# Kernel optimization log

Hardware: AMD Instinct MI355X
Metric: run time of the kernel (lower is better)

## Reference

```python
import jax, jax.numpy as jnp
import numpy as np

N = 50000      # nodes
E = 800000     # edges (avg degree 16)
F_IN = 100     # num_node_features
H = 64         # hidden
C = 18         # num_class
L = 2          # num_layers (extra GINConv blocks after first_conv)
BN_EPS = 1e-5


def setup_inputs() -> dict:
    key = jax.random.key(0)
    ks = jax.random.split(key, 12)
    s = 0.05  # weight init scale
    return {
        "x": jax.random.normal(ks[0], (N, F_IN), dtype=jnp.float32),
        "edge_index": jax.random.randint(ks[1], (2, E), 0, N, dtype=jnp.int32),
        # learnable eps per GINConv (train_eps=True, init 0): [first, layer0, layer1]
        "eps": jnp.zeros((L + 1,), jnp.float32),
        # first_conv MLP: Linear(F_IN,H) -> ReLU -> Linear(H,H)
        "fW1": jax.random.normal(ks[2], (F_IN, H), jnp.float32) * s,
        "fb1": jnp.zeros((H,), jnp.float32),
        "fW2": jax.random.normal(ks[3], (H, H), jnp.float32) * s,
        "fb2": jnp.zeros((H,), jnp.float32),
        # per-layer MLPs, stacked over L layers
        "W1s": jax.random.normal(ks[4], (L, H, H), jnp.float32) * s,
        "b1s": jnp.zeros((L, H), jnp.float32),
        "W2s": jax.random.normal(ks[5], (L, H, H), jnp.float32) * s,
        "b2s": jnp.zeros((L, H), jnp.float32),
        # BatchNorm1d params for first_bn + L bns (eval mode: running stats)
        "bn_gamma": jnp.ones((L + 1, H), jnp.float32),
        "bn_beta": jnp.zeros((L + 1, H), jnp.float32),
        "bn_mean": jnp.zeros((L + 1, H), jnp.float32),
        "bn_var": jnp.ones((L + 1, H), jnp.float32),
        # readout linears
        "lin1_W": jax.random.normal(ks[6], (H, H), jnp.float32) * s,
        "lin1_b": jnp.zeros((H,), jnp.float32),
        "lin2_W": jax.random.normal(ks[7], (H, C), jnp.float32) * s,
        "lin2_b": jnp.zeros((C,), jnp.float32),
    }


def _mlp(h, W1, b1, W2, b2):
    return jnp.maximum(h @ W1 + b1, 0.0) @ W2 + b2


def _gin_conv(x, src, dst, eps, W1, b1, W2, b2):
    # sum aggregation of source features into destination nodes
    agg = jax.ops.segment_sum(x[src], dst, num_segments=N)  # [N, d]
    return _mlp((1.0 + eps) * x + agg, W1, b1, W2, b2)


def _bn_eval(h, g, b, m, v):
    return (h - m) * jax.lax.rsqrt(v + BN_EPS) * g + b


def reference(x, edge_index, eps, fW1, fb1, fW2, fb2, W1s, b1s, W2s, b2s,
              bn_gamma, bn_beta, bn_mean, bn_var, lin1_W, lin1_b, lin2_W, lin2_b):
    src, dst = edge_index[0], edge_index[1]
    h = jnp.maximum(_gin_conv(x, src, dst, eps[0], fW1, fb1, fW2, fb2), 0.0)
    h = _bn_eval(h, bn_gamma[0], bn_beta[0], bn_mean[0], bn_var[0])
    for i in range(L):
        h = jnp.maximum(_gin_conv(h, src, dst, eps[i + 1],
                                  W1s[i], b1s[i], W2s[i], b2s[i]), 0.0)
        h = _bn_eval(h, bn_gamma[i + 1], bn_beta[i + 1], bn_mean[i + 1], bn_var[i + 1])
    h = jnp.maximum(h @ lin1_W + lin1_b, 0.0)
    # dropout is identity in eval mode
    h = h @ lin2_W + lin2_b
    return jax.nn.log_softmax(h, axis=-1)
```

## Files before the change

kernel.cpp:

```cpp
#include <hip/hip_runtime.h>
#include <math.h>

#define NN 50000
#define EE 800000
#define FIN 100
#define HH 64
#define CC 18
#define PD 68
#define TB 782
#define NB 49

__global__ __launch_bounds__(256) void k_count(const int* __restrict__ ei,
                                               int* __restrict__ counts) {
  for (int e = blockIdx.x * 256 + threadIdx.x; e < EE; e += gridDim.x * 256)
    atomicAdd(&counts[ei[EE + e]], 1);
}

__device__ __forceinline__ void load4_guard(const int* __restrict__ a, int i4,
                                            int& c0, int& c1, int& c2,
                                            int& c3) {
  if (i4 + 3 < NN) {
    int4 v = *reinterpret_cast<const int4*>(a + i4);
    c0 = v.x; c1 = v.y; c2 = v.z; c3 = v.w;
  } else {
    c0 = (i4 < NN) ? a[i4] : 0;
    c1 = (i4 + 1 < NN) ? a[i4 + 1] : 0;
    c2 = (i4 + 2 < NN) ? a[i4 + 2] : 0;
    c3 = (i4 + 3 < NN) ? a[i4 + 3] : 0;
  }
}

__global__ __launch_bounds__(256) void k_bsum(const int* __restrict__ counts,
                                              int* __restrict__ bsum) {
  __shared__ int ws[4];
  int t = threadIdx.x, lane = t & 63, wid = t >> 6;
  int i4 = blockIdx.x * 1024 + t * 4;
  int c0, c1, c2, c3;
  load4_guard(counts, i4, c0, c1, c2, c3);
  int s = c0 + c1 + c2 + c3;
#pragma unroll
  for (int m = 32; m >= 1; m >>= 1) s += __shfl_xor(s, m);
  if (lane == 0) ws[wid] = s;
  __syncthreads();
  if (t == 0) bsum[blockIdx.x] = ws[0] + ws[1] + ws[2] + ws[3];
}

__global__ __launch_bounds__(64) void k_bscan(const int* __restrict__ bsum,
                                              int* __restrict__ boff,
                                              int* __restrict__ rowptr) {
  int lane = threadIdx.x;
  int v = (lane < NB) ? bsum[lane] : 0;
  int x = v;
#pragma unroll
  for (int off = 1; off < 64; off <<= 1) {
    int y = __shfl_up(x, off);
    if (lane >= off) x += y;
  }
  if (lane < NB) boff[lane] = x - v;
  if (lane == NB - 1) rowptr[NN] = x;
}

__global__ __launch_bounds__(256) void k_rowptr(const int* __restrict__ counts,
                                                const int* __restrict__ boff,
                                                int* __restrict__ rowptr,
                                                int* __restrict__ cursor) {
  __shared__ int wtot[4];
  int t = threadIdx.x, lane = t & 63, wid = t >> 6;
  int i4 = blockIdx.x * 1024 + t * 4;
  int c0, c1, c2, c3;
  load4_guard(counts, i4, c0, c1, c2, c3);
  int s = c0 + c1 + c2 + c3;
  int x = s;
#pragma unroll
  for (int off = 1; off < 64; off <<= 1) {
    int y = __shfl_up(x, off);
    if (lane >= off) x += y;
  }
  if (lane == 63) wtot[wid] = x;
  __syncthreads();
  int base = boff[blockIdx.x];
  for (int w = 0; w < wid; ++w) base += wtot[w];
  int p = base + x - s;
  int p0 = p, p1 = p0 + c0, p2 = p1 + c1, p3 = p2 + c2;
  if (i4 + 3 < NN) {
    *reinterpret_cast<int4*>(rowptr + i4) = make_int4(p0, p1, p2, p3);
    *reinterpret_cast<int4*>(cursor + i4) = make_int4(p0, p1, p2, p3);
  } else {
    if (i4 < NN) { rowptr[i4] = p0; cursor[i4] = p0; }
    if (i4 + 1 < NN) { rowptr[i4 + 1] = p1; cursor[i4 + 1] = p1; }
    if (i4 + 2 < NN) { rowptr[i4 + 2] = p2; cursor[i4 + 2] = p2; }
  }
}

__global__ __launch_bounds__(256) void k_fill(const int* __restrict__ ei,
                                              int* __restrict__ cursor,
                                              int* __restrict__ eidx) {
  int e2 = (blockIdx.x * 256 + threadIdx.x) * 2;
  if (e2 >= EE) return;
  int2 sv = *reinterpret_cast<const int2*>(ei + e2);
  int2 dv = *reinterpret_cast<const int2*>(ei + EE + e2);
  eidx[atomicAdd(&cursor[dv.x], 1)] = sv.x;
  eidx[atomicAdd(&cursor[dv.y], 1)] = sv.y;
}

__global__ __launch_bounds__(256) void k_gather(
    const float* __restrict__ feat, const int* __restrict__ rowptr,
    const int* __restrict__ eidx, const float* __restrict__ epsv,
    float* __restrict__ zout) {
  int t = threadIdx.x;
  int grp = t >> 4, c4 = t & 15;
  int n = blockIdx.x * 16 + grp;
  if (n >= NN) return;
  float e0 = 1.f + epsv[0];
  int beg = rowptr[n], end = rowptr[n + 1];
  const float* fp = feat + c4 * 4;
  float4 self = *reinterpret_cast<const float4*>(fp + n * HH);
  float ax = e0 * self.x, ay = e0 * self.y, az = e0 * self.z,
        aw = e0 * self.w;
  int i = beg;
  int s0, s1, s2, s3, s4, s5, s6, s7;
  if (i + 8 <= end) {
    s0 = eidx[i + 0]; s1 = eidx[i + 1]; s2 = eidx[i + 2]; s3 = eidx[i + 3];
    s4 = eidx[i + 4]; s5 = eidx[i + 5]; s6 = eidx[i + 6]; s7 = eidx[i + 7];
  }
  while (i + 8 <= end) {
    float4 v0 = *reinterpret_cast<const float4*>(fp + s0 * HH);
    float4 v1 = *reinterpret_cast<const float4*>(fp + s1 * HH);
    float4 v2 = *reinterpret_cast<const float4*>(fp + s2 * HH);
    float4 v3 = *reinterpret_cast<const float4*>(fp + s3 * HH);
    float4 v4 = *reinterpret_cast<const float4*>(fp + s4 * HH);
    float4 v5 = *reinterpret_cast<const float4*>(fp + s5 * HH);
    float4 v6 = *reinterpret_cast<const float4*>(fp + s6 * HH);
    float4 v7 = *reinterpret_cast<const float4*>(fp + s7 * HH);
    int in2 = i + 8;
    if (in2 + 8 <= end) {
      s0 = eidx[in2 + 0]; s1 = eidx[in2 + 1];
      s2 = eidx[in2 + 2]; s3 = eidx[in2 + 3];
      s4 = eidx[in2 + 4]; s5 = eidx[in2 + 5];
      s6 = eidx[in2 + 6]; s7 = eidx[in2 + 7];
    }
    ax += ((v0.x + v1.x) + (v2.x + v3.x)) + ((v4.x + v5.x) + (v6.x + v7.x));
    ay += ((v0.y + v1.y) + (v2.y + v3.y)) + ((v4.y + v5.y) + (v6.y + v7.y));
    az += ((v0.z + v1.z) + (v2.z + v3.z)) + ((v4.z + v5.z) + (v6.z + v7.z));
    aw += ((v0.w + v1.w) + (v2.w + v3.w)) + ((v4.w + v5.w) + (v6.w + v7.w));
    i = in2;
  }
  for (; i < end; ++i) {
    float4 v = *reinterpret_cast<const float4*>(fp + eidx[i] * HH);
    ax += v.x; ay += v.y; az += v.z; aw += v.w;
  }
  *reinterpret_cast<float4*>(zout + n * HH + c4 * 4) =
      make_float4(ax, ay, az, aw);
}

__device__ __forceinline__ void fma4(float4& a, const float4 z,
                                     const float4 w0, const float4 w1,
                                     const float4 w2, const float4 w3) {
  a.x = fmaf(z.x, w0.x, a.x); a.x = fmaf(z.y, w1.x, a.x);
  a.x = fmaf(z.z, w2.x, a.x); a.x = fmaf(z.w, w3.x, a.x);
  a.y = fmaf(z.x, w0.y, a.y); a.y = fmaf(z.y, w1.y, a.y);
  a.y = fmaf(z.z, w2.y, a.y); a.y = fmaf(z.w, w3.y, a.y);
  a.z = fmaf(z.x, w0.z, a.z); a.z = fmaf(z.y, w1.z, a.z);
  a.z = fmaf(z.z, w2.z, a.z); a.z = fmaf(z.w, w3.z, a.z);
  a.w = fmaf(z.x, w0.w, a.w); a.w = fmaf(z.y, w1.w, a.w);
  a.w = fmaf(z.z, w2.w, a.w); a.w = fmaf(z.w, w3.w, a.w);
}

__device__ __forceinline__ void gemm_rc(const float* __restrict__ Zs,
                                        const float* __restrict__ Ws, int c4,
                                        int nl, float4 acc[4]) {
  for (int k4 = 0; k4 < 16; ++k4) {
    float4 w0 = *reinterpret_cast<const float4*>(Ws + (k4 * 4 + 0) * HH + c4 * 4);
    float4 w1 = *reinterpret_cast<const float4*>(Ws + (k4 * 4 + 1) * HH + c4 * 4);
    float4 w2 = *reinterpret_cast<const float4*>(Ws + (k4 * 4 + 2) * HH + c4 * 4);
    float4 w3 = *reinterpret_cast<const float4*>(Ws + (k4 * 4 + 3) * HH + c4 * 4);
#pragma unroll
    for (int q = 0; q < 4; ++q) {
      float4 z = *reinterpret_cast<const float4*>(Zs + (nl * 4 + q) * PD + k4 * 4);
      fma4(acc[q], z, w0, w1, w2, w3);
    }
  }
}

__global__ __launch_bounds__(256) void k_gemm_first(
    const float* __restrict__ x, const float* __restrict__ W,
    float* __restrict__ p) {
  __shared__ float Ws[FIN * HH];
  __shared__ float xs[64 * FIN];
  int t = threadIdx.x;
  int n0 = blockIdx.x * 64;
  for (int i4 = t * 4; i4 < FIN * HH; i4 += 1024)
    *reinterpret_cast<float4*>(Ws + i4) =
        *reinterpret_cast<const float4*>(W + i4);
  for (int i4 = t * 4; i4 < 64 * FIN; i4 += 1024) {
    int r = i4 / FIN, c = i4 - r * FIN;
    int n = n0 + r;
    float4 v = make_float4(0.f, 0.f, 0.f, 0.f);
    if (n < NN) v = *reinterpret_cast<const float4*>(x + n * FIN + c);
    *reinterpret_cast<float4*>(xs + i4) = v;
  }
  __syncthreads();
  int c4 = t & 15, nl = t >> 4;
  float4 acc[4];
#pragma unroll
  for (int q = 0; q < 4; ++q) acc[q] = make_float4(0.f, 0.f, 0.f, 0.f);
  for (int k4 = 0; k4 < FIN / 4; ++k4) {
    float4 w0 = *reinterpret_cast<const float4*>(Ws + (k4 * 4 + 0) * HH + c4 * 4);
    float4 w1 = *reinterpret_cast<const float4*>(Ws + (k4 * 4 + 1) * HH + c4 * 4);
    float4 w2 = *reinterpret_cast<const float4*>(Ws + (k4 * 4 + 2) * HH + c4 * 4);
    float4 w3 = *reinterpret_cast<const float4*>(Ws + (k4 * 4 + 3) * HH + c4 * 4);
#pragma unroll
    for (int q = 0; q < 4; ++q) {
      float4 z = *reinterpret_cast<const float4*>(xs + (nl * 4 + q) * FIN + k4 * 4);
      fma4(acc[q], z, w0, w1, w2, w3);
    }
  }
#pragma unroll
  for (int q = 0; q < 4; ++q) {
    int n = n0 + nl * 4 + q;
    if (n < NN) *reinterpret_cast<float4*>(p + n * HH + c4 * 4) = acc[q];
  }
}

__global__ __launch_bounds__(256) void k_mlp_first(
    const float* __restrict__ zbuf, const float* __restrict__ b1,
    const float* __restrict__ W2, const float* __restrict__ b2,
    const float* __restrict__ g, const float* __restrict__ be,
    const float* __restrict__ mu, const float* __restrict__ var,
    float* __restrict__ out) {
  __shared__ float Zs[64 * PD];
  __shared__ float W2s[HH * HH];
  int t = threadIdx.x;
  int n0 = blockIdx.x * 64;
  for (int i4 = t * 4; i4 < HH * HH; i4 += 1024)
    *reinterpret_cast<float4*>(W2s + i4) =
        *reinterpret_cast<const float4*>(W2 + i4);
  for (int i4 = t * 4; i4 < HH * HH; i4 += 1024) {
    int r = i4 >> 6, c = i4 & 63;
    int n = n0 + r;
    float4 z4 = make_float4(0.f, 0.f, 0.f, 0.f);
    if (n < NN) {
      float4 zv = *reinterpret_cast<const float4*>(zbuf + n * HH + c);
      float4 bv = *reinterpret_cast<const float4*>(b1 + c);
      z4.x = fmaxf(zv.x + bv.x, 0.f);
      z4.y = fmaxf(zv.y + bv.y, 0.f);
      z4.z = fmaxf(zv.z + bv.z, 0.f);
      z4.w = fmaxf(zv.w + bv.w, 0.f);
    }
    *reinterpret_cast<float4*>(Zs + r * PD + c) = z4;
  }
  __syncthreads();
  int c4 = t & 15, nl = t >> 4;
  float4 b2v = *reinterpret_cast<const float4*>(b2 + c4 * 4);
  float4 acc[4];
#pragma unroll
  for (int q = 0; q < 4; ++q) acc[q] = b2v;
  gemm_rc(Zs, W2s, c4, nl, acc);
  float4 gv = *reinterpret_cast<const float4*>(g + c4 * 4);
  float4 bev = *reinterpret_cast<const float4*>(be + c4 * 4);
  float4 muv = *reinterpret_cast<const float4*>(mu + c4 * 4);
  float4 vav = *reinterpret_cast<const float4*>(var + c4 * 4);
  float4 sj, bj;
  sj.x = gv.x * rsqrtf(vav.x + 1e-5f); bj.x = bev.x - muv.x * sj.x;
  sj.y = gv.y * rsqrtf(vav.y + 1e-5f); bj.y = bev.y - muv.y * sj.y;
  sj.z = gv.z * rsqrtf(vav.z + 1e-5f); bj.z = bev.z - muv.z * sj.z;
  sj.w = gv.w * rsqrtf(vav.w + 1e-5f); bj.w = bev.w - muv.w * sj.w;
#pragma unroll
  for (int q = 0; q < 4; ++q) {
    int n = n0 + nl * 4 + q;
    if (n < NN) {
      float4 o;
      o.x = fmaf(fmaxf(acc[q].x, 0.f), sj.x, bj.x);
      o.y = fmaf(fmaxf(acc[q].y, 0.f), sj.y, bj.y);
      o.z = fmaf(fmaxf(acc[q].z, 0.f), sj.z, bj.z);
      o.w = fmaf(fmaxf(acc[q].w, 0.f), sj.w, bj.w);
      *reinterpret_cast<float4*>(out + n * HH + c4 * 4) = o;
    }
  }
}

__global__ __launch_bounds__(256) void k_mlp_layer(
    const float* __restrict__ zbuf, const float* __restrict__ W1,
    const float* __restrict__ b1, const float* __restrict__ W2,
    const float* __restrict__ b2, const float* __restrict__ g,
    const float* __restrict__ be, const float* __restrict__ mu,
    const float* __restrict__ var, float* __restrict__ out) {
  __shared__ float Zs[64 * PD];
  __shared__ float W1s[HH * HH];
  __shared__ float W2s[HH * HH];
  int t = threadIdx.x;
  int n0 = blockIdx.x * 64;
  for (int i4 = t * 4; i4 < HH * HH; i4 += 1024) {
    *reinterpret_cast<float4*>(W1s + i4) =
        *reinterpret_cast<const float4*>(W1 + i4);
    *reinterpret_cast<float4*>(W2s + i4) =
        *reinterpret_cast<const float4*>(W2 + i4);
  }
  for (int i4 = t * 4; i4 < HH * HH; i4 += 1024) {
    int r = i4 >> 6, c = i4 & 63;
    int n = n0 + r;
    float4 z4 = make_float4(0.f, 0.f, 0.f, 0.f);
    if (n < NN) z4 = *reinterpret_cast<const float4*>(zbuf + n * HH + c);
    *reinterpret_cast<float4*>(Zs + r * PD + c) = z4;
  }
  __syncthreads();
  int c4 = t & 15, nl = t >> 4;
  float4 b1v = *reinterpret_cast<const float4*>(b1 + c4 * 4);
  float4 acc[4];
#pragma unroll
  for (int q = 0; q < 4; ++q) acc[q] = b1v;
  gemm_rc(Zs, W1s, c4, nl, acc);
  __syncthreads();
#pragma unroll
  for (int q = 0; q < 4; ++q) {
    float4 tq;
    tq.x = fmaxf(acc[q].x, 0.f); tq.y = fmaxf(acc[q].y, 0.f);
    tq.z = fmaxf(acc[q].z, 0.f); tq.w = fmaxf(acc[q].w, 0.f);
    *reinterpret_cast<float4*>(Zs + (nl * 4 + q) * PD + c4 * 4) = tq;
  }
  __syncthreads();
  float4 b2v = *reinterpret_cast<const float4*>(b2 + c4 * 4);
#pragma unroll
  for (int q = 0; q < 4; ++q) acc[q] = b2v;
  gemm_rc(Zs, W2s, c4, nl, acc);
  float4 gv = *reinterpret_cast<const float4*>(g + c4 * 4);
  float4 bev = *reinterpret_cast<const float4*>(be + c4 * 4);
  float4 muv = *reinterpret_cast<const float4*>(mu + c4 * 4);
  float4 vav = *reinterpret_cast<const float4*>(var + c4 * 4);
  float4 sj, bj;
  sj.x = gv.x * rsqrtf(vav.x + 1e-5f); bj.x = bev.x - muv.x * sj.x;
  sj.y = gv.y * rsqrtf(vav.y + 1e-5f); bj.y = bev.y - muv.y * sj.y;
  sj.z = gv.z * rsqrtf(vav.z + 1e-5f); bj.z = bev.z - muv.z * sj.z;
  sj.w = gv.w * rsqrtf(vav.w + 1e-5f); bj.w = bev.w - muv.w * sj.w;
#pragma unroll
  for (int q = 0; q < 4; ++q) {
    int n = n0 + nl * 4 + q;
    if (n < NN) {
      float4 o;
      o.x = fmaf(fmaxf(acc[q].x, 0.f), sj.x, bj.x);
      o.y = fmaf(fmaxf(acc[q].y, 0.f), sj.y, bj.y);
      o.z = fmaf(fmaxf(acc[q].z, 0.f), sj.z, bj.z);
      o.w = fmaf(fmaxf(acc[q].w, 0.f), sj.w, bj.w);
      *reinterpret_cast<float4*>(out + n * HH + c4 * 4) = o;
    }
  }
}

__global__ __launch_bounds__(256) void k_readout(
    const float* __restrict__ h, const float* __restrict__ W1,
    const float* __restrict__ b1, const float* __restrict__ W2,
    const float* __restrict__ b2, float* __restrict__ out) {
  __shared__ float Zs[64 * PD];
  __shared__ float W1s[HH * HH];
  __shared__ float W2s[HH * CC + 64];
  int t = threadIdx.x;
  int n0 = blockIdx.x * 64;
  for (int i4 = t * 4; i4 < HH * HH; i4 += 1024)
    *reinterpret_cast<float4*>(W1s + i4) =
        *reinterpret_cast<const float4*>(W1 + i4);
  for (int i = t; i < HH * CC + 64; i += 256)
    W2s[i] = (i < HH * CC) ? W2[i] : 0.f;
  for (int i4 = t * 4; i4 < HH * HH; i4 += 1024) {
    int r = i4 >> 6, c = i4 & 63;
    int n = n0 + r;
    float4 z4 = make_float4(0.f, 0.f, 0.f, 0.f);
    if (n < NN) z4 = *reinterpret_cast<const float4*>(h + n * HH + c);
    *reinterpret_cast<float4*>(Zs + r * PD + c) = z4;
  }
  __syncthreads();
  int j = t & 63, nl = t >> 6;
  float b1j = b1[j];
  float b2j = (j < CC) ? b2[j] : 0.f;
  float acc[16];
#pragma unroll
  for (int q = 0; q < 16; ++q) acc[q] = b1j;
  for (int k4 = 0; k4 < 16; ++k4) {
    float w0 = W1s[(k4 * 4 + 0) * HH + j];
    float w1 = W1s[(k4 * 4 + 1) * HH + j];
    float w2 = W1s[(k4 * 4 + 2) * HH + j];
    float w3 = W1s[(k4 * 4 + 3) * HH + j];
#pragma unroll
    for (int q = 0; q < 16; ++q) {
      float4 z = *reinterpret_cast<const float4*>(Zs + (nl + q * 4) * PD + k4 * 4);
      acc[q] = fmaf(z.x, w0, acc[q]);
      acc[q] = fmaf(z.y, w1, acc[q]);
      acc[q] = fmaf(z.z, w2, acc[q]);
      acc[q] = fmaf(z.w, w3, acc[q]);
    }
  }
  __syncthreads();
#pragma unroll
  for (int q = 0; q < 16; ++q)
    Zs[(nl + q * 4) * PD + j] = fmaxf(acc[q], 0.f);
  __syncthreads();
#pragma unroll
  for (int q = 0; q < 16; ++q) acc[q] = b2j;
  for (int k4 = 0; k4 < 16; ++k4) {
    float w0 = W2s[(k4 * 4 + 0) * CC + j];
    float w1 = W2s[(k4 * 4 + 1) * CC + j];
    float w2 = W2s[(k4 * 4 + 2) * CC + j];
    float w3 = W2s[(k4 * 4 + 3) * CC + j];
#pragma unroll
    for (int q = 0; q < 16; ++q) {
      float4 z = *reinterpret_cast<const float4*>(Zs + (nl + q * 4) * PD + k4 * 4);
      acc[q] = fmaf(z.x, w0, acc[q]);
      acc[q] = fmaf(z.y, w1, acc[q]);
      acc[q] = fmaf(z.z, w2, acc[q]);
      acc[q] = fmaf(z.w, w3, acc[q]);
    }
  }
#pragma unroll
  for (int q = 0; q < 16; ++q) {
    float o = acc[q];
    float om = (j < CC) ? o : -3.4e38f;
    float mx = om;
#pragma unroll
    for (int m = 32; m >= 1; m >>= 1) mx = fmaxf(mx, __shfl_xor(mx, m));
    float ex = (j < CC) ? expf(o - mx) : 0.f;
    float sm = ex;
#pragma unroll
    for (int m = 32; m >= 1; m >>= 1) sm += __shfl_xor(sm, m);
    int n = n0 + nl + q * 4;
    if (n < NN && j < CC) out[n * CC + j] = o - mx - logf(sm);
  }
}

extern "C" void kernel_launch(void* const* d_in, const int* in_sizes, int n_in,
                              void* d_out, int out_size, void* d_ws,
                              size_t ws_size, hipStream_t stream) {
  const float* x = (const float*)d_in[0];
  const int* ei = (const int*)d_in[1];
  const float* eps = (const float*)d_in[2];
  const float* fW1 = (const float*)d_in[3];
  const float* fb1 = (const float*)d_in[4];
  const float* fW2 = (const float*)d_in[5];
  const float* fb2 = (const float*)d_in[6];
  const float* W1s = (const float*)d_in[7];
  const float* b1s = (const float*)d_in[8];
  const float* W2s = (const float*)d_in[9];
  const float* b2s = (const float*)d_in[10];
  const float* bn_g = (const float*)d_in[11];
  const float* bn_b = (const float*)d_in[12];
  const float* bn_m = (const float*)d_in[13];
  const float* bn_v = (const float*)d_in[14];
  const float* l1W = (const float*)d_in[15];
  const float* l1b = (const float*)d_in[16];
  const float* l2W = (const float*)d_in[17];
  const float* l2b = (const float*)d_in[18];
  float* out = (float*)d_out;

  int* eidx = (int*)d_ws;
  int* rowptr = eidx + EE;
  int* boff = rowptr + NN + 1;
  int* bsum = boff + NB;
  size_t int_elems = (size_t)EE + NN + 1 + 2 * NB;
  size_t f_off = (int_elems + 3) & ~(size_t)3;
  const size_t NH = (size_t)NN * HH;
  float* buf0 = (float*)d_ws + f_off;
  float* buf1 = buf0 + NH;
  float* buf2 = buf1 + NH;
  int* counts = (int*)buf1;
  int* cursor = counts + NN;

  hipMemsetAsync(counts, 0, NN * sizeof(int), stream);
  k_count<<<2048, 256, 0, stream>>>(ei, counts);
  k_bsum<<<NB, 256, 0, stream>>>(counts, bsum);
  k_bscan<<<1, 64, 0, stream>>>(bsum, boff, rowptr);
  k_rowptr<<<NB, 256, 0, stream>>>(counts, boff, rowptr, cursor);
  k_fill<<<(EE / 2 + 255) / 256, 256, 0, stream>>>(ei, cursor, eidx);

  k_gemm_first<<<TB, 256, 0, stream>>>(x, fW1, buf0);

  k_gather<<<(NN + 15) / 16, 256, 0, stream>>>(buf0, rowptr, eidx, eps + 0,
                                               buf1);
  k_mlp_first<<<TB, 256, 0, stream>>>(buf1, fb1, fW2, fb2, bn_g, bn_b, bn_m,
                                      bn_v, buf2);
  k_gather<<<(NN + 15) / 16, 256, 0, stream>>>(buf2, rowptr, eidx, eps + 1,
                                               buf1);
  k_mlp_layer<<<TB, 256, 0, stream>>>(buf1, W1s, b1s, W2s, b2s, bn_g + HH,
                                      bn_b + HH, bn_m + HH, bn_v + HH, buf0);
  k_gather<<<(NN + 15) / 16, 256, 0, stream>>>(buf0, rowptr, eidx, eps + 2,
                                               buf1);
  k_mlp_layer<<<TB, 256, 0, stream>>>(buf1, W1s + HH * HH, b1s + HH,
                                      W2s + HH * HH, b2s + HH, bn_g + 2 * HH,
                                      bn_b + 2 * HH, bn_m + 2 * HH,
                                      bn_v + 2 * HH, buf2);
  k_readout<<<TB, 256, 0, stream>>>(buf2, l1W, l1b, l2W, l2b, out);
}
```

Measured before the change: 416.4 us.

## Store gathered node features in bf16 and fold block scan into rowptr

Node features that the neighbour gathers read (first GEMM output and the MLP outputs that feed the next layer) are now stored as bf16. This halves the bytes fetched by the random-access gather kernels, which read about 16 neighbour rows per node. Accumulation still happens in fp32, but rounding the stored activations to bf16 can shift accuracy against the fp32 reference. Separately, the single-block scan kernel is removed: each rowptr block now sums the preceding block totals itself. The fill kernel also processes four edges per thread instead of two.

Result: faster. 375.1 us (-9.9%).

```diff
diff --git a/kernel.cpp b/kernel.cpp
--- a/kernel.cpp
+++ b/kernel.cpp
@@ -9,6 +9,18 @@
 #define PD 68
 #define TB 782
 #define NB 49
+
+typedef unsigned short u16;
+typedef unsigned int u32;
+
+__device__ __forceinline__ u16 f2bf(float f) {
+  u32 u = __float_as_uint(f);
+  u = (u + 0x7fffu + ((u >> 16) & 1u)) >> 16;
+  return (u16)u;
+}
+__device__ __forceinline__ float bf2f(u16 s) {
+  return __uint_as_float(((u32)s) << 16);
+}
 
 __global__ __launch_bounds__(256) void k_count(const int* __restrict__ ei,
                                                int* __restrict__ counts) {
@@ -45,27 +57,22 @@
   if (t == 0) bsum[blockIdx.x] = ws[0] + ws[1] + ws[2] + ws[3];
 }
 
-__global__ __launch_bounds__(64) void k_bscan(const int* __restrict__ bsum,
-                                              int* __restrict__ boff,
-                                              int* __restrict__ rowptr) {
-  int lane = threadIdx.x;
-  int v = (lane < NB) ? bsum[lane] : 0;
-  int x = v;
-#pragma unroll
-  for (int off = 1; off < 64; off <<= 1) {
-    int y = __shfl_up(x, off);
-    if (lane >= off) x += y;
-  }
-  if (lane < NB) boff[lane] = x - v;
-  if (lane == NB - 1) rowptr[NN] = x;
-}
-
 __global__ __launch_bounds__(256) void k_rowptr(const int* __restrict__ counts,
-                                                const int* __restrict__ boff,
+                                                const int* __restrict__ bsum,
                                                 int* __restrict__ rowptr,
                                                 int* __restrict__ cursor) {
+  __shared__ int redw[4];
   __shared__ int wtot[4];
+  __shared__ int sbase;
   int t = threadIdx.x, lane = t & 63, wid = t >> 6;
+  int sb = (t < blockIdx.x) ? bsum[t] : 0;
+#pragma unroll
+  for (int m = 32; m >= 1; m >>= 1) sb += __shfl_xor(sb, m);
+  if (lane == 0) redw[wid] = sb;
+  __syncthreads();
+  if (t == 0) sbase = redw[0] + redw[1] + redw[2] + redw[3];
+  __syncthreads();
+  int base0 = sbase;
   int i4 = blockIdx.x * 1024 + t * 4;
   int c0, c1, c2, c3;
   load4_guard(counts, i4, c0, c1, c2, c3);
@@ -78,7 +85,7 @@
   }
   if (lane == 63) wtot[wid] = x;
   __syncthreads();
-  int base = boff[blockIdx.x];
+  int base = base0;
   for (int w = 0; w < wid; ++w) base += wtot[w];
   int p = base + x - s;
   int p0 = p, p1 = p0 + c0, p2 = p1 + c1, p3 = p2 + c2;
@@ -90,21 +97,24 @@
     if (i4 + 1 < NN) { rowptr[i4 + 1] = p1; cursor[i4 + 1] = p1; }
     if (i4 + 2 < NN) { rowptr[i4 + 2] = p2; cursor[i4 + 2] = p2; }
   }
+  if (i4 + 4 == NN) rowptr[NN] = p3 + c3;
 }
 
 __global__ __launch_bounds__(256) void k_fill(const int* __restrict__ ei,
                                               int* __restrict__ cursor,
                                               int* __restrict__ eidx) {
-  int e2 = (blockIdx.x * 256 + threadIdx.x) * 2;
-  if (e2 >= EE) return;
-  int2 sv = *reinterpret_cast<const int2*>(ei + e2);
-  int2 dv = *reinterpret_cast<const int2*>(ei + EE + e2);
+  int e4 = (blockIdx.x * 256 + threadIdx.x) * 4;
+  if (e4 >= EE) return;
+  int4 sv = *reinterpret_cast<const int4*>(ei + e4);
+  int4 dv = *reinterpret_cast<const int4*>(ei + EE + e4);
   eidx[atomicAdd(&cursor[dv.x], 1)] = sv.x;
   eidx[atomicAdd(&cursor[dv.y], 1)] = sv.y;
+  eidx[atomicAdd(&cursor[dv.z], 1)] = sv.z;
+  eidx[atomicAdd(&cursor[dv.w], 1)] = sv.w;
 }
 
 __global__ __launch_bounds__(256) void k_gather(
-    const float* __restrict__ feat, const int* __restrict__ rowptr,
+    const u16* __restrict__ feat, const int* __restrict__ rowptr,
     const int* __restrict__ eidx, const float* __restrict__ epsv,
     float* __restrict__ zout) {
   int t = threadIdx.x;
@@ -113,10 +123,10 @@
   if (n >= NN) return;
   float e0 = 1.f + epsv[0];
   int beg = rowptr[n], end = rowptr[n + 1];
-  const float* fp = feat + c4 * 4;
-  float4 self = *reinterpret_cast<const float4*>(fp + n * HH);
-  float ax = e0 * self.x, ay = e0 * self.y, az = e0 * self.z,
-        aw = e0 * self.w;
+  const u16* fp = feat + c4 * 4;
+  ushort4 sf = *reinterpret_cast<const ushort4*>(fp + (size_t)n * HH);
+  float ax = e0 * bf2f(sf.x), ay = e0 * bf2f(sf.y), az = e0 * bf2f(sf.z),
+        aw = e0 * bf2f(sf.w);
   int i = beg;
   int s0, s1, s2, s3, s4, s5, s6, s7;
   if (i + 8 <= end) {
@@ -124,14 +134,14 @@
     s4 = eidx[i + 4]; s5 = eidx[i + 5]; s6 = eidx[i + 6]; s7 = eidx[i + 7];
   }
   while (i + 8 <= end) {
-    float4 v0 = *reinterpret_cast<const float4*>(fp + s0 * HH);
-    float4 v1 = *reinterpret_cast<const float4*>(fp + s1 * HH);
-    float4 v2 = *reinterpret_cast<const float4*>(fp + s2 * HH);
-    float4 v3 = *reinterpret_cast<const float4*>(fp + s3 * HH);
-    float4 v4 = *reinterpret_cast<const float4*>(fp + s4 * HH);
-    float4 v5 = *reinterpret_cast<const float4*>(fp + s5 * HH);
-    float4 v6 = *reinterpret_cast<const float4*>(fp + s6 * HH);
-    float4 v7 = *reinterpret_cast<const float4*>(fp + s7 * HH);
+    ushort4 v0 = *reinterpret_cast<const ushort4*>(fp + (size_t)s0 * HH);
+    ushort4 v1 = *reinterpret_cast<const ushort4*>(fp + (size_t)s1 * HH);
+    ushort4 v2 = *reinterpret_cast<const ushort4*>(fp + (size_t)s2 * HH);
+    ushort4 v3 = *reinterpret_cast<const ushort4*>(fp + (size_t)s3 * HH);
+    ushort4 v4 = *reinterpret_cast<const ushort4*>(fp + (size_t)s4 * HH);
+    ushort4 v5 = *reinterpret_cast<const ushort4*>(fp + (size_t)s5 * HH);
+    ushort4 v6 = *reinterpret_cast<const ushort4*>(fp + (size_t)s6 * HH);
+    ushort4 v7 = *reinterpret_cast<const ushort4*>(fp + (size_t)s7 * HH);
     int in2 = i + 8;
     if (in2 + 8 <= end) {
       s0 = eidx[in2 + 0]; s1 = eidx[in2 + 1];
@@ -139,17 +149,21 @@
       s4 = eidx[in2 + 4]; s5 = eidx[in2 + 5];
       s6 = eidx[in2 + 6]; s7 = eidx[in2 + 7];
     }
-    ax += ((v0.x + v1.x) + (v2.x + v3.x)) + ((v4.x + v5.x) + (v6.x + v7.x));
-    ay += ((v0.y + v1.y) + (v2.y + v3.y)) + ((v4.y + v5.y) + (v6.y + v7.y));
-    az += ((v0.z + v1.z) + (v2.z + v3.z)) + ((v4.z + v5.z) + (v6.z + v7.z));
-    aw += ((v0.w + v1.w) + (v2.w + v3.w)) + ((v4.w + v5.w) + (v6.w + v7.w));
+    ax += ((bf2f(v0.x) + bf2f(v1.x)) + (bf2f(v2.x) + bf2f(v3.x))) +
+          ((bf2f(v4.x) + bf2f(v5.x)) + (bf2f(v6.x) + bf2f(v7.x)));
+    ay += ((bf2f(v0.y) + bf2f(v1.y)) + (bf2f(v2.y) + bf2f(v3.y))) +
+          ((bf2f(v4.y) + bf2f(v5.y)) + (bf2f(v6.y) + bf2f(v7.y)));
+    az += ((bf2f(v0.z) + bf2f(v1.z)) + (bf2f(v2.z) + bf2f(v3.z))) +
+          ((bf2f(v4.z) + bf2f(v5.z)) + (bf2f(v6.z) + bf2f(v7.z)));
+    aw += ((bf2f(v0.w) + bf2f(v1.w)) + (bf2f(v2.w) + bf2f(v3.w))) +
+          ((bf2f(v4.w) + bf2f(v5.w)) + (bf2f(v6.w) + bf2f(v7.w)));
     i = in2;
   }
   for (; i < end; ++i) {
-    float4 v = *reinterpret_cast<const float4*>(fp + eidx[i] * HH);
-    ax += v.x; ay += v.y; az += v.z; aw += v.w;
-  }
-  *reinterpret_cast<float4*>(zout + n * HH + c4 * 4) =
+    ushort4 v = *reinterpret_cast<const ushort4*>(fp + (size_t)eidx[i] * HH);
+    ax += bf2f(v.x); ay += bf2f(v.y); az += bf2f(v.z); aw += bf2f(v.w);
+  }
+  *reinterpret_cast<float4*>(zout + (size_t)n * HH + c4 * 4) =
       make_float4(ax, ay, az, aw);
 }
 
@@ -184,7 +198,7 @@
 
 __global__ __launch_bounds__(256) void k_gemm_first(
     const float* __restrict__ x, const float* __restrict__ W,
-    float* __restrict__ p) {
+    u16* __restrict__ p) {
   __shared__ float Ws[FIN * HH];
   __shared__ float xs[64 * FIN];
   int t = threadIdx.x;
@@ -218,7 +232,12 @@
 #pragma unroll
   for (int q = 0; q < 4; ++q) {
     int n = n0 + nl * 4 + q;
-    if (n < NN) *reinterpret_cast<float4*>(p + n * HH + c4 * 4) = acc[q];
+    if (n < NN) {
+      ushort4 ub;
+      ub.x = f2bf(acc[q].x); ub.y = f2bf(acc[q].y);
+      ub.z = f2bf(acc[q].z); ub.w = f2bf(acc[q].w);
+      *reinterpret_cast<ushort4*>(p + (size_t)n * HH + c4 * 4) = ub;
+    }
   }
 }
 
@@ -227,7 +246,7 @@
     const float* __restrict__ W2, const float* __restrict__ b2,
     const float* __restrict__ g, const float* __restrict__ be,
     const float* __restrict__ mu, const float* __restrict__ var,
-    float* __restrict__ out) {
+    u16* __restrict__ out) {
   __shared__ float Zs[64 * PD];
   __shared__ float W2s[HH * HH];
   int t = threadIdx.x;
@@ -240,7 +259,7 @@
     int n = n0 + r;
     float4 z4 = make_float4(0.f, 0.f, 0.f, 0.f);
     if (n < NN) {
-      float4 zv = *reinterpret_cast<const float4*>(zbuf + n * HH + c);
+      float4 zv = *reinterpret_cast<const float4*>(zbuf + (size_t)n * HH + c);
       float4 bv = *reinterpret_cast<const float4*>(b1 + c);
       z4.x = fmaxf(zv.x + bv.x, 0.f);
       z4.y = fmaxf(zv.y + bv.y, 0.f);
@@ -269,22 +288,23 @@
   for (int q = 0; q < 4; ++q) {
     int n = n0 + nl * 4 + q;
     if (n < NN) {
-      float4 o;
-      o.x = fmaf(fmaxf(acc[q].x, 0.f), sj.x, bj.x);
-      o.y = fmaf(fmaxf(acc[q].y, 0.f), sj.y, bj.y);
-      o.z = fmaf(fmaxf(acc[q].z, 0.f), sj.z, bj.z);
-      o.w = fmaf(fmaxf(acc[q].w, 0.f), sj.w, bj.w);
-      *reinterpret_cast<float4*>(out + n * HH + c4 * 4) = o;
-    }
-  }
-}
-
+      ushort4 ub;
+      ub.x = f2bf(fmaf(fmaxf(acc[q].x, 0.f), sj.x, bj.x));
+      ub.y = f2bf(fmaf(fmaxf(acc[q].y, 0.f), sj.y, bj.y));
+      ub.z = f2bf(fmaf(fmaxf(acc[q].z, 0.f), sj.z, bj.z));
+      ub.w = f2bf(fmaf(fmaxf(acc[q].w, 0.f), sj.w, bj.w));
+      *reinterpret_cast<ushort4*>(out + (size_t)n * HH + c4 * 4) = ub;
+    }
+  }
+}
+
+template <bool BF>
 __global__ __launch_bounds__(256) void k_mlp_layer(
     const float* __restrict__ zbuf, const float* __restrict__ W1,
     const float* __restrict__ b1, const float* __restrict__ W2,
     const float* __restrict__ b2, const float* __restrict__ g,
     const float* __restrict__ be, const float* __restrict__ mu,
-    const float* __restrict__ var, float* __restrict__ out) {
+    const float* __restrict__ var, void* __restrict__ outp) {
   __shared__ float Zs[64 * PD];
   __shared__ float W1s[HH * HH];
   __shared__ float W2s[HH * HH];
@@ -300,7 +320,7 @@
     int r = i4 >> 6, c = i4 & 63;
     int n = n0 + r;
     float4 z4 = make_float4(0.f, 0.f, 0.f, 0.f);
-    if (n < NN) z4 = *reinterpret_cast<const float4*>(zbuf + n * HH + c);
+    if (n < NN) z4 = *reinterpret_cast<const float4*>(zbuf + (size_t)n * HH + c);
     *reinterpret_cast<float4*>(Zs + r * PD + c) = z4;
   }
   __syncthreads();
@@ -341,7 +361,14 @@
       o.y = fmaf(fmaxf(acc[q].y, 0.f), sj.y, bj.y);
       o.z = fmaf(fmaxf(acc[q].z, 0.f), sj.z, bj.z);
       o.w = fmaf(fmaxf(acc[q].w, 0.f), sj.w, bj.w);
-      *reinterpret_cast<float4*>(out + n * HH + c4 * 4) = o;
+      if constexpr (BF) {
+        ushort4 ub;
+        ub.x = f2bf(o.x); ub.y = f2bf(o.y);
+        ub.z = f2bf(o.z); ub.w = f2bf(o.w);
+        *reinterpret_cast<ushort4*>((u16*)outp + (size_t)n * HH + c4 * 4) = ub;
+      } else {
+        *reinterpret_cast<float4*>((float*)outp + (size_t)n * HH + c4 * 4) = o;
+      }
     }
   }
 }
@@ -364,7 +391,7 @@
     int r = i4 >> 6, c = i4 & 63;
     int n = n0 + r;
     float4 z4 = make_float4(0.f, 0.f, 0.f, 0.f);
-    if (n < NN) z4 = *reinterpret_cast<const float4*>(h + n * HH + c);
+    if (n < NN) z4 = *reinterpret_cast<const float4*>(h + (size_t)n * HH + c);
     *reinterpret_cast<float4*>(Zs + r * PD + c) = z4;
   }
   __syncthreads();
@@ -451,39 +478,39 @@
 
   int* eidx = (int*)d_ws;
   int* rowptr = eidx + EE;
-  int* boff = rowptr + NN + 1;
-  int* bsum = boff + NB;
-  size_t int_elems = (size_t)EE + NN + 1 + 2 * NB;
+  int* bsum = rowptr + NN + 1;
+  size_t int_elems = (size_t)EE + NN + 1 + NB;
   size_t f_off = (int_elems + 3) & ~(size_t)3;
   const size_t NH = (size_t)NN * HH;
-  float* buf0 = (float*)d_ws + f_off;
-  float* buf1 = buf0 + NH;
-  float* buf2 = buf1 + NH;
-  int* counts = (int*)buf1;
+  float* zbuf = (float*)d_ws + f_off;
+  u16* hbf = (u16*)(zbuf + NH);
+  float* h2 = zbuf + NH + NH / 2;
+  int* counts = (int*)zbuf;
   int* cursor = counts + NN;
 
   hipMemsetAsync(counts, 0, NN * sizeof(int), stream);
   k_count<<<2048, 256, 0, stream>>>(ei, counts);
   k_bsum<<<NB, 256, 0, stream>>>(counts, bsum);
-  k_bscan<<<1, 64, 0, stream>>>(bsum, boff, rowptr);
-  k_rowptr<<<NB, 256, 0, stream>>>(counts, boff, rowptr, cursor);
-  k_fill<<<(EE / 2 + 255) / 256, 256, 0, stream>>>(ei, cursor, eidx);
-
-  k_gemm_first<<<TB, 256, 0, stream>>>(x, fW1, buf0);
-
-  k_gather<<<(NN + 15) / 16, 256, 0, stream>>>(buf0, rowptr, eidx, eps + 0,
-                                               buf1);
-  k_mlp_first<<<TB, 256, 0, stream>>>(buf1, fb1, fW2, fb2, bn_g, bn_b, bn_m,
-                                      bn_v, buf2);
-  k_gather<<<(NN + 15) / 16, 256, 0, stream>>>(buf2, rowptr, eidx, eps + 1,
-                                               buf1);
-  k_mlp_layer<<<TB, 256, 0, stream>>>(buf1, W1s, b1s, W2s, b2s, bn_g + HH,
-                                      bn_b + HH, bn_m + HH, bn_v + HH, buf0);
-  k_gather<<<(NN + 15) / 16, 256, 0, stream>>>(buf0, rowptr, eidx, eps + 2,
-                                               buf1);
-  k_mlp_layer<<<TB, 256, 0, stream>>>(buf1, W1s + HH * HH, b1s + HH,
-                                      W2s + HH * HH, b2s + HH, bn_g + 2 * HH,
-                                      bn_b + 2 * HH, bn_m + 2 * HH,
-                                      bn_v + 2 * HH, buf2);
-  k_readout<<<TB, 256, 0, stream>>>(buf2, l1W, l1b, l2W, l2b, out);
-}
+  k_rowptr<<<NB, 256, 0, stream>>>(counts, bsum, rowptr, cursor);
+  k_fill<<<(EE / 4 + 255) / 256, 256, 0, stream>>>(ei, cursor, eidx);
+
+  k_gemm_first<<<TB, 256, 0, stream>>>(x, fW1, hbf);
+
+  k_gather<<<(NN + 15) / 16, 256, 0, stream>>>(hbf, rowptr, eidx, eps + 0,
+                                               zbuf);
+  k_mlp_first<<<TB, 256, 0, stream>>>(zbuf, fb1, fW2, fb2, bn_g, bn_b, bn_m,
+                                      bn_v, hbf);
+  k_gather<<<(NN + 15) / 16, 256, 0, stream>>>(hbf, rowptr, eidx, eps + 1,
+                                               zbuf);
+  k_mlp_layer<true><<<TB, 256, 0, stream>>>(zbuf, W1s, b1s, W2s, b2s,
+                                            bn_g + HH, bn_b + HH, bn_m + HH,
+                                            bn_v + HH, (void*)hbf);
+  k_gather<<<(NN + 15) / 16, 256, 0, stream>>>(hbf, rowptr, eidx, eps + 2,
+                                               zbuf);
+  k_mlp_layer<false><<<TB, 256, 0, stream>>>(zbuf, W1s + HH * HH, b1s + HH,
+                                             W2s + HH * HH, b2s + HH,
+                                             bn_g + 2 * HH, bn_b + 2 * HH,
+                                             bn_m + 2 * HH, bn_v + 2 * HH,
+                                             (void*)h2);
+  k_readout<<<TB, 256, 0, stream>>>(h2, l1W, l1b, l2W, l2b, out);
+}
```
